# Kernel optimization log

Hardware: AMD Instinct MI355X
Metric: run time of the kernel (lower is better)

Reference implementation:

```python
import jax, jax.numpy as jnp
import numpy as np
from jax import lax

# ---- configuration (matches init_kwargs / input_specs) ----
N = 16384          # number of input points
F_IN = 64          # input feature dim
RATIO = 0.25       # fps ratio
M = int(N * RATIO) # number of sampled centers = 4096
RADIUS = 0.2       # radius for neighbor search
K = 64             # max_num_neighbors
F_HID = 64
F_OUT = 128


def _glorot(key, shape):
    fan_in = shape[0]
    return jax.random.normal(key, shape, jnp.float32) / jnp.sqrt(jnp.float32(fan_in))


def setup_inputs() -> dict:
    key = jax.random.key(0)
    ks = jax.random.split(key, 6)
    x = jax.random.normal(ks[0], (N, F_IN), jnp.float32)
    pos = jax.random.normal(ks[1], (N, 3), jnp.float32)
    batch = jnp.zeros((N,), jnp.int32)  # single point cloud
    # PointNet++ SA conv MLP: [F_IN+3 -> 64 -> 64 -> 128]
    W1 = _glorot(ks[2], (F_IN + 3, F_HID))
    b1 = jnp.zeros((F_HID,), jnp.float32)
    W2 = _glorot(ks[3], (F_HID, F_HID))
    b2 = jnp.zeros((F_HID,), jnp.float32)
    W3 = _glorot(ks[4], (F_HID, F_OUT))
    b3 = jnp.zeros((F_OUT,), jnp.float32)
    return {"x": x, "pos": pos, "batch": batch,
            "W1": W1, "b1": b1, "W2": W2, "b2": b2, "W3": W3, "b3": b3}


def fps(pos, m):
    """Farthest point sampling: returns m indices into pos [N,3]."""
    n = pos.shape[0]

    def step(carry, _):
        min_d2, last = carry
        d2 = jnp.sum((pos - pos[last]) ** 2, axis=-1)   # [N]
        min_d2 = jnp.minimum(min_d2, d2)
        nxt = jnp.argmax(min_d2).astype(jnp.int32)
        return (min_d2, nxt), last

    init = (jnp.full((n,), jnp.inf, pos.dtype), jnp.int32(0))
    _, idx = lax.scan(step, init, None, length=m)
    return idx  # [m]


def radius_neighbors(pos, pos_s, batch, batch_s, r, k):
    """For each center, k nearest neighbors within radius r (same batch).
    Returns nbr indices [M,K] and validity mask [M,K]."""
    d2 = jnp.sum((pos_s[:, None, :] - pos[None, :, :]) ** 2, axis=-1)  # [M,N]
    ok = (batch_s[:, None] == batch[None, :]) & (d2 <= r * r)
    score = jnp.where(ok, d2, jnp.inf)
    neg_vals, nbr = lax.top_k(-score, k)                # smallest distances first
    valid = jnp.isfinite(neg_vals)
    return nbr, valid


def reference(x, pos, batch, W1, b1, W2, b2, W3, b3):
    idx = fps(pos, M)                   # [M]
    pos_s = pos[idx]                    # [M,3]
    batch_s = batch[idx]                # [M]
    nbr, valid = radius_neighbors(pos, pos_s, batch, batch_s, RADIUS, K)
    # gather neighbor features and relative positions
    rel = pos[nbr] - pos_s[:, None, :]                      # [M,K,3]
    h = jnp.concatenate([x[nbr], rel], axis=-1)             # [M,K,F_IN+3]
    # per-edge MLP (PointNetConv message)
    h = jax.nn.relu(h @ W1 + b1)
    h = jax.nn.relu(h @ W2 + b2)
    h = jax.nn.relu(h @ W3 + b3)                            # [M,K,F_OUT]
    # max aggregation over valid neighbors (center is always its own neighbor)
    h = jnp.where(valid[..., None], h, -jnp.inf)
    out = jnp.max(h, axis=1)                                # [M,F_OUT]
    return out, pos_s, batch_s
```

## Files before the change

kernel.cpp:

```cpp
#include <hip/hip_runtime.h>

#define N_PTS 16384
#define M_CTR 4096
#define K_NBR 64
#define F_OUT 128
#define CAP   256
#define FS    68
#define NCELL 4096
#define NBKT  512

__device__ __forceinline__ float d2_exact(float ax, float ay, float az,
                                          float bx, float by, float bz) {
  float dx = __fsub_rn(ax, bx);
  float dy = __fsub_rn(ay, by);
  float dz = __fsub_rn(az, bz);
  return __fadd_rn(__fadd_rn(__fmul_rn(dx, dx), __fmul_rn(dy, dy)),
                   __fmul_rn(dz, dz));
}

__device__ __forceinline__ unsigned long long wave_max_u64(unsigned long long v) {
  int lo = (int)(unsigned)v;
  int hi = (int)(unsigned)(v >> 32);
#define DPPSTEP64(ctrl, rm)                                                    \
  {                                                                            \
    int tlo = __builtin_amdgcn_update_dpp(lo, lo, ctrl, rm, 0xf, false);       \
    int thi = __builtin_amdgcn_update_dpp(hi, hi, ctrl, rm, 0xf, false);       \
    unsigned long long cur =                                                   \
        ((unsigned long long)(unsigned)hi << 32) | (unsigned)lo;               \
    unsigned long long oth =                                                   \
        ((unsigned long long)(unsigned)thi << 32) | (unsigned)tlo;             \
    if (oth > cur) { lo = tlo; hi = thi; }                                     \
  }
  DPPSTEP64(0x111, 0xf) DPPSTEP64(0x112, 0xf) DPPSTEP64(0x114, 0xf)
  DPPSTEP64(0x118, 0xf) DPPSTEP64(0x142, 0xa) DPPSTEP64(0x143, 0xc)
#undef DPPSTEP64
  const unsigned rlo = (unsigned)__builtin_amdgcn_readlane(lo, 63);
  const unsigned rhi = (unsigned)__builtin_amdgcn_readlane(hi, 63);
  return ((unsigned long long)rhi << 32) | rlo;
}

__device__ __forceinline__ unsigned long long bucket_bfly_max_u64(
    unsigned long long red) {
  {
    int lo = (int)(unsigned)red, hi = (int)(unsigned)(red >> 32);
    int tlo = __builtin_amdgcn_update_dpp(lo, lo, 0xB1, 0xf, 0xf, false);
    int thi = __builtin_amdgcn_update_dpp(hi, hi, 0xB1, 0xf, 0xf, false);
    unsigned long long o =
        ((unsigned long long)(unsigned)thi << 32) | (unsigned)tlo;
    if (o > red) red = o;
    lo = (int)(unsigned)red; hi = (int)(unsigned)(red >> 32);
    tlo = __builtin_amdgcn_update_dpp(lo, lo, 0x4E, 0xf, 0xf, false);
    thi = __builtin_amdgcn_update_dpp(hi, hi, 0x4E, 0xf, 0xf, false);
    o = ((unsigned long long)(unsigned)thi << 32) | (unsigned)tlo;
    if (o > red) red = o;
  }
#pragma unroll
  for (int mH = 4; mH < 32; mH <<= 1) {
    const unsigned olo = (unsigned)__shfl_xor((int)(unsigned)red, mH);
    const unsigned ohi = (unsigned)__shfl_xor((int)(unsigned)(red >> 32), mH);
    const unsigned long long o = ((unsigned long long)ohi << 32) | olo;
    if (o > red) red = o;
  }
  return red;
}

__global__ void __launch_bounds__(1024) prep_bbox_kernel(const float* __restrict__ pos,
                                                         float* __restrict__ bbox,
                                                         int* __restrict__ hist) {
  const int tid = threadIdx.x;
  __shared__ float sred[6][16];
  float mn[3] = {INFINITY, INFINITY, INFINITY};
  float mx[3] = {-INFINITY, -INFINITY, -INFINITY};
  for (int p = tid; p < N_PTS; p += 1024) {
#pragma unroll
    for (int d = 0; d < 3; ++d) {
      float v = pos[3 * p + d];
      mn[d] = fminf(mn[d], v);
      mx[d] = fmaxf(mx[d], v);
    }
  }
#pragma unroll
  for (int off = 32; off > 0; off >>= 1) {
#pragma unroll
    for (int d = 0; d < 3; ++d) {
      mn[d] = fminf(mn[d], __shfl_xor(mn[d], off));
      mx[d] = fmaxf(mx[d], __shfl_xor(mx[d], off));
    }
  }
  if ((tid & 63) == 0) {
    const int w = tid >> 6;
#pragma unroll
    for (int d = 0; d < 3; ++d) { sred[d][w] = mn[d]; sred[3 + d][w] = mx[d]; }
  }
  __syncthreads();
  if (tid == 0) {
#pragma unroll
    for (int d = 0; d < 3; ++d) {
      float a = sred[d][0], b = sred[3 + d][0];
      for (int w = 1; w < 16; ++w) { a = fminf(a, sred[d][w]); b = fmaxf(b, sred[3 + d][w]); }
      bbox[d] = a; bbox[3 + d] = b;
    }
  }
  for (int i = tid; i < NCELL; i += 1024) hist[i] = 0;
}

__device__ __forceinline__ int spread4(int v) {
  return (v & 1) | ((v & 2) << 2) | ((v & 4) << 4) | ((v & 8) << 6);
}

__global__ void __launch_bounds__(256) prep_cell_kernel(const float* __restrict__ pos,
                                                        const float* __restrict__ bbox,
                                                        int* __restrict__ cellid,
                                                        int* __restrict__ hist) {
  const int p = blockIdx.x * 256 + threadIdx.x;
  const float x = pos[3 * p], y = pos[3 * p + 1], z = pos[3 * p + 2];
  const float x0 = bbox[0], y0 = bbox[1], z0 = bbox[2];
  const float sx = 16.0f / fmaxf(bbox[3] - x0, 1e-20f);
  const float sy = 16.0f / fmaxf(bbox[4] - y0, 1e-20f);
  const float sz = 16.0f / fmaxf(bbox[5] - z0, 1e-20f);
  int cx = min(15, (int)((x - x0) * sx));
  int cy = min(15, (int)((y - y0) * sy));
  int cz = min(15, (int)((z - z0) * sz));
  const int c = spread4(cx) | (spread4(cy) << 1) | (spread4(cz) << 2);
  cellid[p] = c;
  atomicAdd(&hist[c], 1);
}

__global__ void __launch_bounds__(1024) prep_scan_kernel(const int* __restrict__ hist,
                                                         int* __restrict__ cursor) {
  __shared__ int tsum[1024];
  const int t = threadIdx.x;
  const int v0 = hist[4 * t + 0], v1 = hist[4 * t + 1];
  const int v2 = hist[4 * t + 2], v3 = hist[4 * t + 3];
  const int s = v0 + v1 + v2 + v3;
  int acc = s;
  tsum[t] = acc;
  __syncthreads();
  for (int off = 1; off < 1024; off <<= 1) {
    int add = (t >= off) ? tsum[t - off] : 0;
    __syncthreads();
    acc += add;
    tsum[t] = acc;
    __syncthreads();
  }
  int base = acc - s;
  cursor[4 * t + 0] = base;
  cursor[4 * t + 1] = base + v0;
  cursor[4 * t + 2] = base + v0 + v1;
  cursor[4 * t + 3] = base + v0 + v1 + v2;
}

__global__ void __launch_bounds__(256) prep_scatter_kernel(const float* __restrict__ pos,
                                                           const int* __restrict__ cellid,
                                                           int* __restrict__ cursor,
                                                           float4* __restrict__ gxyz) {
  const int p = blockIdx.x * 256 + threadIdx.x;
  const int c = cellid[p];
  const int dst = atomicAdd(&cursor[c], 1);
  gxyz[dst] = make_float4(pos[3 * p + 0], pos[3 * p + 1], pos[3 * p + 2],
                          __int_as_float(p));
}

__global__ void __launch_bounds__(64) prep_bktbox_kernel(const float4* __restrict__ gxyz,
                                                         float* __restrict__ gbox) {
  const int lane = threadIdx.x;
  const float4 q = gxyz[blockIdx.x * 64 + lane];
  float mnx = q.x, mxx = q.x, mny = q.y, mxy = q.y, mnz = q.z, mxz = q.z;
#pragma unroll
  for (int off = 16; off > 0; off >>= 1) {
    mnx = fminf(mnx, __shfl_xor(mnx, off)); mxx = fmaxf(mxx, __shfl_xor(mxx, off));
    mny = fminf(mny, __shfl_xor(mny, off)); mxy = fmaxf(mxy, __shfl_xor(mxy, off));
    mnz = fminf(mnz, __shfl_xor(mnz, off)); mxz = fmaxf(mxz, __shfl_xor(mxz, off));
  }
  if ((lane & 31) == 0) {
    const int b = blockIdx.x * 2 + (lane >> 5);
    gbox[b * 8 + 0] = mnx; gbox[b * 8 + 1] = mxx;
    gbox[b * 8 + 2] = mny; gbox[b * 8 + 3] = mxy;
    gbox[b * 8 + 4] = mnz; gbox[b * 8 + 5] = mxz;
    gbox[b * 8 + 6] = 0.0f; gbox[b * 8 + 7] = 0.0f;
  }
}

__global__ void __launch_bounds__(512) fps_bucket_kernel(
    const float* __restrict__ pos, const float4* __restrict__ gxyz,
    const float* __restrict__ gbox,
    int* __restrict__ idx_out, float* __restrict__ pos_s_out,
    float* __restrict__ batch_s_out) {
  __shared__ float s_md[N_PTS];
  __shared__ unsigned long long s_pk[NBKT];
  __shared__ float4 s_wxyz[NBKT];
  __shared__ int s_wl[NBKT];
  __shared__ int s_cnt[2];
  __shared__ int s_sidx[M_CTR];
  const int tid = threadIdx.x;
  const int lane = tid & 63, wave = tid >> 6;

  for (int i = tid; i < N_PTS; i += 512) s_md[i] = INFINITY;
  const float bx0 = gbox[tid * 8 + 0], bx1 = gbox[tid * 8 + 1];
  const float by0 = gbox[tid * 8 + 2], by1 = gbox[tid * 8 + 3];
  const float bz0 = gbox[tid * 8 + 4], bz1 = gbox[tid * 8 + 5];
  unsigned long long mpk = ((unsigned long long)0x7f800000u << 32);
  s_pk[tid] = mpk;
  if (tid < 2) s_cnt[tid] = 0;
  float cx = pos[0], cy = pos[1], cz = pos[2];
  int cIdx = 0;
  __syncthreads();

  for (int t = 0; t < M_CTR; ++t) {
    if (tid == 0) s_sidx[t] = cIdx;
    if (t == M_CTR - 1) break;
    const int par = t & 1;

    const float rMax = __uint_as_float((unsigned)(mpk >> 32));
    float dxl = fmaxf(fmaxf(bx0 - cx, cx - bx1), 0.0f);
    float dyl = fmaxf(fmaxf(by0 - cy, cy - by1), 0.0f);
    float dzl = fmaxf(fmaxf(bz0 - cz, cz - bz1), 0.0f);
    const bool flag = (dxl * dxl + dyl * dyl + dzl * dzl) * 0.99999f < rMax;
    const unsigned long long ball = __ballot(flag);
    int base = 0;
    if (lane == 0) base = atomicAdd(&s_cnt[par], __popcll(ball));
    base = __builtin_amdgcn_readfirstlane(base);
    if (flag) {
      const int pre = __popcll(ball & ((1ull << lane) - 1ull));
      s_wl[base + pre] = tid;
    }
    __syncthreads();
    if (tid == 0) s_cnt[par ^ 1] = 0;

    const int nf = s_cnt[par];
    const int total = nf << 5;
    for (int bi = 0; bi < total; bi += 512) {
      const int idx = bi + tid;
      if (idx < total) {
        const int b = s_wl[idx >> 5];
        const int p = (b << 5) | (idx & 31);
        const float4 q = gxyz[p];
        const float nmd = fminf(s_md[p], d2_exact(q.x, q.y, q.z, cx, cy, cz));
        s_md[p] = nmd;
        const unsigned long long own =
            ((unsigned long long)__float_as_uint(nmd) << 32) |
            ((unsigned long long)(16383u - (unsigned)__float_as_int(q.w)) << 14) |
            (unsigned)p;
        const unsigned long long red = bucket_bfly_max_u64(own);
        if (own == red) {
          s_pk[b] = red;
          s_wxyz[b] = make_float4(q.x, q.y, q.z, 0.0f);
        }
      }
    }
    __syncthreads();

    unsigned long long loc = 0ULL;
#pragma unroll
    for (int k = 0; k < 8; ++k) {
      const unsigned long long v = s_pk[(k << 6) | lane];
      if (k == wave) mpk = v;
      if (v > loc) loc = v;
    }
    const unsigned long long bpk = wave_max_u64(loc);
    cIdx = 16383 - (int)((bpk >> 14) & 16383u);
    const int posn = (int)(bpk & 16383u);
    const float4 cq = s_wxyz[posn >> 5];
    cx = cq.x; cy = cq.y; cz = cq.z;
  }
  __syncthreads();
  for (int i = tid; i < M_CTR; i += 512) {
    const int si = s_sidx[i];
    idx_out[i] = si;
    pos_s_out[3 * i + 0] = pos[3 * si + 0];
    pos_s_out[3 * i + 1] = pos[3 * si + 1];
    pos_s_out[3 * i + 2] = pos[3 * si + 2];
    batch_s_out[i] = 0.0f;
  }
}

__global__ void __launch_bounds__(256) nbr_kernel(const float* __restrict__ pos,
                                                  const int* __restrict__ idx,
                                                  int* __restrict__ nbr) {
  const int m = blockIdx.x, tid = threadIdx.x;
  __shared__ int s_cnt;
  __shared__ float s_d2[CAP];
  __shared__ int s_idx[CAP];
  if (tid == 0) s_cnt = 0;
  const int cen = idx[m];
  const float cx = pos[3 * cen + 0], cy = pos[3 * cen + 1], cz = pos[3 * cen + 2];
  __syncthreads();
  const float RR = 0.04f;
  for (int i = 0; i < N_PTS / 256; ++i) {
    const int p = tid + 256 * i;
    float d2 = d2_exact(pos[3 * p], pos[3 * p + 1], pos[3 * p + 2], cx, cy, cz);
    if (d2 <= RR) {
      int slot = atomicAdd(&s_cnt, 1);
      if (slot < CAP) { s_d2[slot] = d2; s_idx[slot] = p; }
    }
  }
  __syncthreads();
  const int cnt = s_cnt;
  if (cnt <= K_NBR) {
    if (tid < K_NBR) nbr[m * K_NBR + tid] = (tid < cnt) ? s_idx[tid] : cen;
  } else {
    const int n = cnt < CAP ? cnt : CAP;
    if (tid >= n) { s_d2[tid] = INFINITY; s_idx[tid] = 0x7fffffff; }
    __syncthreads();
    for (int k = 2; k <= CAP; k <<= 1) {
      for (int j = k >> 1; j > 0; j >>= 1) {
        const int ixj = tid ^ j;
        if (ixj > tid) {
          float da = s_d2[tid], db = s_d2[ixj];
          int ia = s_idx[tid], ib = s_idx[ixj];
          bool gt = (da > db) || (da == db && ia > ib);
          bool asc = ((tid & k) == 0);
          if (gt == asc) {
            s_d2[tid] = db; s_d2[ixj] = da;
            s_idx[tid] = ib; s_idx[ixj] = ia;
          }
        }
        __syncthreads();
      }
    }
    if (tid < K_NBR) nbr[m * K_NBR + tid] = s_idx[tid];
  }
}

__device__ __forceinline__ void mlp_layer(const float (*__restrict__ A)[FS],
                                          const float (*__restrict__ W)[64],
                                          int K, int e0, int c0, float acc[4][4]) {
#pragma unroll
  for (int j = 0; j < 4; ++j)
#pragma unroll
    for (int i = 0; i < 4; ++i) acc[j][i] = W[67][c0 + i];
#pragma unroll 4
  for (int k = 0; k < K; ++k) {
    const float4 w = *(const float4*)&W[k][c0];
    const float a0 = A[e0 + 0][k], a1 = A[e0 + 1][k];
    const float a2 = A[e0 + 2][k], a3 = A[e0 + 3][k];
    acc[0][0] = fmaf(a0, w.x, acc[0][0]); acc[0][1] = fmaf(a0, w.y, acc[0][1]);
    acc[0][2] = fmaf(a0, w.z, acc[0][2]); acc[0][3] = fmaf(a0, w.w, acc[0][3]);
    acc[1][0] = fmaf(a1, w.x, acc[1][0]); acc[1][1] = fmaf(a1, w.y, acc[1][1]);
    acc[1][2] = fmaf(a1, w.z, acc[1][2]); acc[1][3] = fmaf(a1, w.w, acc[1][3]);
    acc[2][0] = fmaf(a2, w.x, acc[2][0]); acc[2][1] = fmaf(a2, w.y, acc[2][1]);
    acc[2][2] = fmaf(a2, w.z, acc[2][2]); acc[2][3] = fmaf(a2, w.w, acc[2][3]);
    acc[3][0] = fmaf(a3, w.x, acc[3][0]); acc[3][1] = fmaf(a3, w.y, acc[3][1]);
    acc[3][2] = fmaf(a3, w.z, acc[3][2]); acc[3][3] = fmaf(a3, w.w, acc[3][3]);
  }
#pragma unroll
  for (int j = 0; j < 4; ++j)
#pragma unroll
    for (int i = 0; i < 4; ++i) acc[j][i] = fmaxf(acc[j][i], 0.0f);
}

__global__ void __launch_bounds__(512) mlp_kernel(
    const float* __restrict__ x, const float* __restrict__ pos,
    const int* __restrict__ nbr, const float* __restrict__ pos_s,
    const float* __restrict__ W1, const float* __restrict__ b1,
    const float* __restrict__ W2, const float* __restrict__ b2,
    const float* __restrict__ W3, const float* __restrict__ b3,
    float* __restrict__ out) {
  __shared__ float Fb[2][64][FS];
  __shared__ float Wb[FS][64];
  __shared__ float Pb[2][16][64];
  __shared__ int s_nbr[128];
  const int t = threadIdx.x;
  const int m0 = blockIdx.x * 2;

  if (t < 128) s_nbr[t] = nbr[m0 * K_NBR + t];
  __syncthreads();

  {
    const int ge = t >> 2, wch = ge >> 6, e = ge & 63, c16 = (t & 3) * 16;
    const int n = s_nbr[ge];
    const float4* src = (const float4*)(x + n * 64 + c16);
    float4* dst = (float4*)(&Fb[wch][e][c16]);
    dst[0] = src[0]; dst[1] = src[1]; dst[2] = src[2]; dst[3] = src[3];
  }
  if (t < 128) {
    const int wch = t >> 6, e = t & 63;
    const int n = s_nbr[t];
    const float cx = pos_s[(m0 + wch) * 3 + 0];
    const float cy = pos_s[(m0 + wch) * 3 + 1];
    const float cz = pos_s[(m0 + wch) * 3 + 2];
    Fb[wch][e][64] = pos[3 * n + 0] - cx;
    Fb[wch][e][65] = pos[3 * n + 1] - cy;
    Fb[wch][e][66] = pos[3 * n + 2] - cz;
    Fb[wch][e][67] = 0.0f;
  }
  for (int i = t; i < 67 * 64; i += 512) ((float*)Wb)[i] = W1[i];
  if (t < 64) Wb[67][t] = b1[t];
  __syncthreads();

  const int wch = t >> 8, tt = t & 255;
  const int e0 = (tt >> 4) << 2, c0 = (tt & 15) << 2;
  float acc[4][4];

  mlp_layer(Fb[wch], Wb, 67, e0, c0, acc);
  __syncthreads();
#pragma unroll
  for (int j = 0; j < 4; ++j)
#pragma unroll
    for (int i = 0; i < 4; ++i) Fb[wch][e0 + j][c0 + i] = acc[j][i];
  for (int i = t; i < 64 * 64; i += 512) ((float*)Wb)[i] = W2[i];
  if (t < 64) Wb[67][t] = b2[t];
  __syncthreads();

  mlp_layer(Fb[wch], Wb, 64, e0, c0, acc);
  __syncthreads();
#pragma unroll
  for (int j = 0; j < 4; ++j)
#pragma unroll
    for (int i = 0; i < 4; ++i) Fb[wch][e0 + j][c0 + i] = acc[j][i];

  for (int h = 0; h < 2; ++h) {
    for (int i = t; i < 64 * 64; i += 512)
      ((float*)Wb)[i] = W3[(i >> 6) * 128 + h * 64 + (i & 63)];
    if (t < 64) Wb[67][t] = b3[h * 64 + t];
    __syncthreads();
    mlp_layer(Fb[wch], Wb, 64, e0, c0, acc);
#pragma unroll
    for (int i = 0; i < 4; ++i) {
      float v = fmaxf(fmaxf(acc[0][i], acc[1][i]), fmaxf(acc[2][i], acc[3][i]));
      Pb[wch][tt >> 4][c0 + i] = v;
    }
    __syncthreads();
    if (tt < 64) {
      float v = Pb[wch][0][tt];
#pragma unroll
      for (int r = 1; r < 16; ++r) v = fmaxf(v, Pb[wch][r][tt]);
      out[(m0 + wch) * F_OUT + h * 64 + tt] = v;
    }
    __syncthreads();
  }
}

extern "C" void kernel_launch(void* const* d_in, const int* in_sizes, int n_in,
                              void* d_out, int out_size, void* d_ws, size_t ws_size,
                              hipStream_t stream) {
  const float* x   = (const float*)d_in[0];
  const float* pos = (const float*)d_in[1];
  const float* W1 = (const float*)d_in[3];
  const float* b1 = (const float*)d_in[4];
  const float* W2 = (const float*)d_in[5];
  const float* b2 = (const float*)d_in[6];
  const float* W3 = (const float*)d_in[7];
  const float* b3 = (const float*)d_in[8];

  float* out     = (float*)d_out;
  float* pos_s   = out + M_CTR * F_OUT;
  float* batch_s = pos_s + M_CTR * 3;

  int*    idx    = (int*)d_ws;
  int*    nbr    = idx + M_CTR;
  float*  bbox   = (float*)(nbr + M_CTR * K_NBR);
  int*    hist   = (int*)(bbox + 8);
  int*    cursor = hist + NCELL;
  int*    cellid = cursor + NCELL;
  float4* gxyz   = (float4*)(cellid + N_PTS);
  float*  gbox   = (float*)hist;

  prep_bbox_kernel<<<1, 1024, 0, stream>>>(pos, bbox, hist);
  prep_cell_kernel<<<N_PTS / 256, 256, 0, stream>>>(pos, bbox, cellid, hist);
  prep_scan_kernel<<<1, 1024, 0, stream>>>(hist, cursor);
  prep_scatter_kernel<<<N_PTS / 256, 256, 0, stream>>>(pos, cellid, cursor, gxyz);
  prep_bktbox_kernel<<<NBKT / 2, 64, 0, stream>>>(gxyz, gbox);
  fps_bucket_kernel<<<1, 512, 0, stream>>>(pos, gxyz, gbox, idx, pos_s, batch_s);
  nbr_kernel<<<M_CTR, 256, 0, stream>>>(pos, idx, nbr);
  mlp_kernel<<<M_CTR / 2, 512, 0, stream>>>(x, pos, nbr, pos_s,
                                            W1, b1, W2, b2, W3, b3, out);
}
```

Measured before the change: 6.070 ms.

## Select two FPS centers per round when runner-up is provably unaffected

```diff
diff --git a/kernel.cpp b/kernel.cpp
--- a/kernel.cpp
+++ b/kernel.cpp
@@ -16,6 +16,10 @@
   float dz = __fsub_rn(az, bz);
   return __fadd_rn(__fadd_rn(__fmul_rn(dx, dx), __fmul_rn(dy, dy)),
                    __fmul_rn(dz, dz));
+}
+
+__device__ __forceinline__ float readlane_f(float v, int ln) {
+  return __int_as_float(__builtin_amdgcn_readlane(__float_as_int(v), ln));
 }
 
 __device__ __forceinline__ unsigned long long wave_max_u64(unsigned long long v) {
@@ -41,27 +45,21 @@
 
 __device__ __forceinline__ unsigned long long bucket_bfly_max_u64(
     unsigned long long red) {
-  {
-    int lo = (int)(unsigned)red, hi = (int)(unsigned)(red >> 32);
-    int tlo = __builtin_amdgcn_update_dpp(lo, lo, 0xB1, 0xf, 0xf, false);
-    int thi = __builtin_amdgcn_update_dpp(hi, hi, 0xB1, 0xf, 0xf, false);
-    unsigned long long o =
-        ((unsigned long long)(unsigned)thi << 32) | (unsigned)tlo;
-    if (o > red) red = o;
-    lo = (int)(unsigned)red; hi = (int)(unsigned)(red >> 32);
-    tlo = __builtin_amdgcn_update_dpp(lo, lo, 0x4E, 0xf, 0xf, false);
-    thi = __builtin_amdgcn_update_dpp(hi, hi, 0x4E, 0xf, 0xf, false);
-    o = ((unsigned long long)(unsigned)thi << 32) | (unsigned)tlo;
-    if (o > red) red = o;
-  }
-#pragma unroll
-  for (int mH = 4; mH < 32; mH <<= 1) {
-    const unsigned olo = (unsigned)__shfl_xor((int)(unsigned)red, mH);
-    const unsigned ohi = (unsigned)__shfl_xor((int)(unsigned)(red >> 32), mH);
-    const unsigned long long o = ((unsigned long long)ohi << 32) | olo;
-    if (o > red) red = o;
-  }
-  return red;
+#define RORSTEP(ctrl)                                                          \
+  {                                                                            \
+    int lo = (int)(unsigned)red, hi = (int)(unsigned)(red >> 32);              \
+    int tlo = __builtin_amdgcn_update_dpp(lo, lo, ctrl, 0xf, 0xf, false);      \
+    int thi = __builtin_amdgcn_update_dpp(hi, hi, ctrl, 0xf, 0xf, false);      \
+    unsigned long long o =                                                     \
+        ((unsigned long long)(unsigned)thi << 32) | (unsigned)tlo;             \
+    if (o > red) red = o;                                                      \
+  }
+  RORSTEP(0x121) RORSTEP(0x122) RORSTEP(0x124) RORSTEP(0x128)
+#undef RORSTEP
+  const unsigned olo = (unsigned)__shfl_xor((int)(unsigned)red, 16);
+  const unsigned ohi = (unsigned)__shfl_xor((int)(unsigned)(red >> 32), 16);
+  const unsigned long long o = ((unsigned long long)ohi << 32) | olo;
+  return (o > red) ? o : red;
 }
 
 __global__ void __launch_bounds__(1024) prep_bbox_kernel(const float* __restrict__ pos,
@@ -202,20 +200,38 @@
   unsigned long long mpk = ((unsigned long long)0x7f800000u << 32);
   s_pk[tid] = mpk;
   if (tid < 2) s_cnt[tid] = 0;
-  float cx = pos[0], cy = pos[1], cz = pos[2];
-  int cIdx = 0;
-  __syncthreads();
-
-  for (int t = 0; t < M_CTR; ++t) {
-    if (tid == 0) s_sidx[t] = cIdx;
-    if (t == M_CTR - 1) break;
-    const int par = t & 1;
+
+  float cxA = pos[0], cyA = pos[1], czA = pos[2];
+  int idA = 0;
+  float cxB = 0.0f, cyB = 0.0f, czB = 0.0f;
+  int idB = 0;
+  bool dual = false;
+  int t = 0, rc = 0;
+  __syncthreads();
+
+  while (true) {
+    if (tid == 0) s_sidx[t] = idA;
+    ++t;
+    if (t >= M_CTR) break;
+    if (dual) {
+      if (tid == 0) s_sidx[t] = idB;
+      ++t;
+      if (t >= M_CTR) break;
+    }
+    const int par = rc & 1;
+    ++rc;
 
     const float rMax = __uint_as_float((unsigned)(mpk >> 32));
-    float dxl = fmaxf(fmaxf(bx0 - cx, cx - bx1), 0.0f);
-    float dyl = fmaxf(fmaxf(by0 - cy, cy - by1), 0.0f);
-    float dzl = fmaxf(fmaxf(bz0 - cz, cz - bz1), 0.0f);
-    const bool flag = (dxl * dxl + dyl * dyl + dzl * dzl) * 0.99999f < rMax;
+    float dxl = fmaxf(fmaxf(bx0 - cxA, cxA - bx1), 0.0f);
+    float dyl = fmaxf(fmaxf(by0 - cyA, cyA - by1), 0.0f);
+    float dzl = fmaxf(fmaxf(bz0 - czA, czA - bz1), 0.0f);
+    bool flag = (dxl * dxl + dyl * dyl + dzl * dzl) * 0.99999f < rMax;
+    if (dual) {
+      float ex = fmaxf(fmaxf(bx0 - cxB, cxB - bx1), 0.0f);
+      float ey = fmaxf(fmaxf(by0 - cyB, cyB - by1), 0.0f);
+      float ez = fmaxf(fmaxf(bz0 - czB, czB - bz1), 0.0f);
+      flag = flag || ((ex * ex + ey * ey + ez * ez) * 0.99999f < rMax);
+    }
     const unsigned long long ball = __ballot(flag);
     int base = 0;
     if (lane == 0) base = atomicAdd(&s_cnt[par], __popcll(ball));
@@ -235,7 +251,8 @@
         const int b = s_wl[idx >> 5];
         const int p = (b << 5) | (idx & 31);
         const float4 q = gxyz[p];
-        const float nmd = fminf(s_md[p], d2_exact(q.x, q.y, q.z, cx, cy, cz));
+        float nmd = fminf(s_md[p], d2_exact(q.x, q.y, q.z, cxA, cyA, czA));
+        if (dual) nmd = fminf(nmd, d2_exact(q.x, q.y, q.z, cxB, cyB, czB));
         s_md[p] = nmd;
         const unsigned long long own =
             ((unsigned long long)__float_as_uint(nmd) << 32) |
@@ -250,18 +267,59 @@
     }
     __syncthreads();
 
+    unsigned long long vv[8];
     unsigned long long loc = 0ULL;
 #pragma unroll
     for (int k = 0; k < 8; ++k) {
-      const unsigned long long v = s_pk[(k << 6) | lane];
-      if (k == wave) mpk = v;
-      if (v > loc) loc = v;
+      const unsigned long long u = s_pk[(k << 6) | lane];
+      vv[k] = u;
+      if (k == wave) mpk = u;
+      if (u > loc) loc = u;
     }
     const unsigned long long bpk = wave_max_u64(loc);
-    cIdx = 16383 - (int)((bpk >> 14) & 16383u);
-    const int posn = (int)(bpk & 16383u);
-    const float4 cq = s_wxyz[posn >> 5];
-    cx = cq.x; cy = cq.y; cz = cq.z;
+    idA = 16383 - (int)((bpk >> 14) & 16383u);
+    const int posn1 = (int)(bpk & 16383u);
+    const int b1 = posn1 >> 5;
+    {
+      const float4 cq = s_wxyz[b1];
+      cxA = cq.x; cyA = cq.y; czA = cq.z;
+    }
+
+    unsigned long long loc2 = 0ULL;
+#pragma unroll
+    for (int k = 0; k < 8; ++k) {
+      const int bb = (k << 6) | lane;
+      const unsigned long long u = (bb == b1) ? 0ULL : vv[k];
+      if (u > loc2) loc2 = u;
+    }
+    const int pp = (b1 << 5) | (lane & 31);
+    const float mdv = s_md[pp];
+    const float4 qq = gxyz[pp];
+    unsigned long long spk =
+        ((unsigned long long)__float_as_uint(mdv) << 32) |
+        ((unsigned long long)(16383u - (unsigned)__float_as_int(qq.w)) << 14) |
+        (unsigned)pp;
+    if (pp == posn1) spk = 0ULL;
+    if (spk > loc2) loc2 = spk;
+    const unsigned long long Rpk = wave_max_u64(loc2);
+    const unsigned hiR = (unsigned)(Rpk >> 32);
+    const int posnR = (int)(Rpk & 16383u);
+    float rx, ry, rz;
+    if ((posnR >> 5) == b1) {
+      const int ln = posnR & 31;
+      rx = readlane_f(qq.x, ln);
+      ry = readlane_f(qq.y, ln);
+      rz = readlane_f(qq.z, ln);
+    } else {
+      const float4 w = s_wxyz[posnR >> 5];
+      rx = w.x; ry = w.y; rz = w.z;
+    }
+    const float dAR = d2_exact(rx, ry, rz, cxA, cyA, czA);
+    dual = (hiR != 0u) && (dAR >= __uint_as_float(hiR));
+    if (dual) {
+      cxB = rx; cyB = ry; czB = rz;
+      idB = 16383 - (int)((Rpk >> 14) & 16383u);
+    }
   }
   __syncthreads();
   for (int i = tid; i < M_CTR; i += 512) {
```

Result: faster. 5.376 ms, median of 3 (-11.4%).
